# Kernel tuning notes

Hardware: AMD Instinct MI355X
Metric: run time of the kernel (lower is better)

Reference implementation:

```python
import jax, jax.numpy as jnp
import numpy as np

WS = 8          # window_size
HEADS = 8
HEAD_DIM = 32
DIM = 256
INNER = HEADS * HEAD_DIM  # 256
STRIDE = 2 * WS - 1       # 15


def _rel_idx_1d():
    # coords of the WS*WS pixels in a window
    coords = np.array([[x, y] for x in range(WS) for y in range(WS)], dtype=np.int32)
    rel = coords[None, :, :] - coords[:, None, :] + (WS - 1)   # [WS^2, WS^2, 2] in [0, 2WS-2]
    idx = rel[:, :, 0] * STRIDE + rel[:, :, 1]
    return jnp.asarray(np.clip(idx, 0, None).reshape(-1), dtype=jnp.int32)

_REL_IDX = _rel_idx_1d()  # [WS^2 * WS^2]


def setup_inputs() -> dict:
    key = jax.random.key(0)
    ks = jax.random.split(key, 5)
    b, l, H, W = 2, 4, 128, 128
    x = jax.random.normal(ks[0], (b, l, H, W, DIM), dtype=jnp.float32)
    W_qkv = jax.random.normal(ks[1], (DIM, 3 * INNER), dtype=jnp.float32) * (DIM ** -0.5)
    W_out = jax.random.normal(ks[2], (INNER, DIM), dtype=jnp.float32) * (INNER ** -0.5)
    b_out = jax.random.normal(ks[3], (DIM,), dtype=jnp.float32) * 0.02
    pos_emb = jax.random.normal(ks[4], (STRIDE, STRIDE), dtype=jnp.float32)
    return {"x": x, "W_qkv": W_qkv, "W_out": W_out, "b_out": b_out, "pos_emb": pos_emb}


def _to_windows(t, b, l, nh, nw):
    # [b,l,H,W,INNER] -> [b,l,heads,nh*nw,WS*WS,head_dim]
    t = t.reshape(b, l, nh, WS, nw, WS, HEADS, HEAD_DIM)
    t = t.transpose(0, 1, 6, 2, 4, 3, 5, 7)  # b l h nh nw ws ws d
    return t.reshape(b, l, HEADS, nh * nw, WS * WS, HEAD_DIM)


def reference(x, W_qkv, W_out, b_out, pos_emb):
    b, l, H, W, _ = x.shape
    nh, nw = H // WS, W // WS
    scale = HEAD_DIM ** -0.5

    qkv = x @ W_qkv                               # [b,l,H,W,3*INNER]
    q, k, v = jnp.split(qkv, 3, axis=-1)
    q = _to_windows(q, b, l, nh, nw)
    k = _to_windows(k, b, l, nh, nw)
    v = _to_windows(v, b, l, nh, nw)

    # per-window attention scores: [b,l,heads,windows,WS^2,WS^2]
    dots = jnp.einsum('blhwid,blhwjd->blhwij', q, k) * scale
    bias = pos_emb.reshape(-1)[_REL_IDX].reshape(WS * WS, WS * WS)
    dots = dots + bias

    attn = jax.nn.softmax(dots, axis=-1)
    out = jnp.einsum('blhwij,blhwjd->blhwid', attn, v)  # [b,l,heads,windows,WS^2,hd]

    # back to [b,l,H,W,INNER]
    out = out.reshape(b, l, HEADS, nh, nw, WS, WS, HEAD_DIM)
    out = out.transpose(0, 1, 3, 5, 4, 6, 2, 7)  # b l nh ws nw ws h d
    out = out.reshape(b, l, nh * WS, nw * WS, INNER)

    return out @ W_out + b_out  # dropout is identity at eval
```

## Files before the change

### kernel.cpp

```cpp
#include <hip/hip_runtime.h>
#include <hip/hip_bf16.h>

typedef short bf16x8 __attribute__((ext_vector_type(8)));
typedef float f32x4  __attribute__((ext_vector_type(4)));
typedef unsigned short u16;
typedef unsigned int u32;

#define MFMA16(a, b, c) __builtin_amdgcn_mfma_f32_16x16x32_bf16((a), (b), (c), 0, 0, 0)

static __device__ __forceinline__ u16 f2b(float f) {
  __hip_bfloat16 h = __float2bfloat16(f);
  return __builtin_bit_cast(u16, h);
}
static __device__ __forceinline__ float b2f(u16 v) {
  unsigned int u = ((unsigned int)v) << 16;
  return __builtin_bit_cast(float, u);
}
static __device__ __forceinline__ u32 pk2(float a, float b) {
  return (u32)f2b(a) | ((u32)f2b(b) << 16);
}

union FragU { uint4 u; bf16x8 v; };

static __device__ __forceinline__ bf16x8 shufx(uint2 lo, uint2 hi,
                                               int sA4, int sB4, bool uh) {
  u32 l0 = (u32)__builtin_amdgcn_ds_bpermute(sA4, (int)lo.x);
  u32 l1 = (u32)__builtin_amdgcn_ds_bpermute(sA4, (int)lo.y);
  u32 h0 = (u32)__builtin_amdgcn_ds_bpermute(sA4, (int)hi.x);
  u32 h1 = (u32)__builtin_amdgcn_ds_bpermute(sA4, (int)hi.y);
  u32 l2 = (u32)__builtin_amdgcn_ds_bpermute(sB4, (int)lo.x);
  u32 l3 = (u32)__builtin_amdgcn_ds_bpermute(sB4, (int)lo.y);
  u32 h2 = (u32)__builtin_amdgcn_ds_bpermute(sB4, (int)hi.x);
  u32 h3 = (u32)__builtin_amdgcn_ds_bpermute(sB4, (int)hi.y);
  FragU f;
  f.u.x = uh ? h0 : l0;  f.u.y = uh ? h1 : l1;
  f.u.z = uh ? h2 : l2;  f.u.w = uh ? h3 : l3;
  return f.v;
}

__global__ void prep(const float* __restrict__ wqkv, const float* __restrict__ wout,
                     const float* __restrict__ pos, u16* __restrict__ wqkT,
                     u16* __restrict__ wvB, u16* __restrict__ woutB,
                     u16* __restrict__ biasQ) {
  const int b = blockIdx.x, t = threadIdx.x;
  const float s = 0.17677669529663689f;
  if (b < 128) {
    int e0 = b * 1024 + t * 4;
#pragma unroll
    for (int i = 0; i < 4; ++i) {
      int e = e0 + i, o = e >> 8, ii = e & 255;
      float v = wqkv[(size_t)ii * 768 + o];
      wqkT[e] = f2b(o < 256 ? v * s : v);
    }
  } else if (b < 192) {
    int e0 = (b - 128) * 1024 + t * 4;
#pragma unroll
    for (int i = 0; i < 4; ++i) {
      int e = e0 + i, frag = e >> 9, w = e & 511, lane = w >> 3, ee = w & 7;
      int k8 = frag >> 4, np = frag & 15;
      int k = k8 * 32 + ((lane >> 4) << 3) + ee;
      int col = 512 + np * 16 + (lane & 15);
      wvB[e] = f2b(wqkv[(size_t)k * 768 + col]);
    }
  } else if (b < 256) {
    int e0 = (b - 192) * 1024 + t * 4;
#pragma unroll
    for (int i = 0; i < 4; ++i) {
      int e = e0 + i, frag = e >> 9, w = e & 511, lane = w >> 3, ee = w & 7;
      int k8 = frag >> 4, np = frag & 15;
      int k = k8 * 32 + ((lane >> 4) << 3) + ee;
      int col = np * 16 + (lane & 15);
      woutB[e] = f2b(wout[(size_t)k * 256 + col]);
    }
  } else {
    int e0 = (b - 256) * 1024 + t * 4;
#pragma unroll
    for (int i = 0; i < 4; ++i) {
      int e = e0 + i, iq = e >> 6, jk = e & 63;
      int ix = iq >> 3, iy = iq & 7, jx = jk >> 3, jy = jk & 7;
      biasQ[e] = f2b(pos[(jx - ix + 7) * 15 + (jy - iy + 7)]);
    }
  }
}

__global__ __launch_bounds__(512, 4)
void winattn(const float* __restrict__ x,
             const u16* __restrict__ wqkT,
             const u16* __restrict__ wvB,
             const u16* __restrict__ woutB,
             const float* __restrict__ b_out,
             const u16* __restrict__ biasQ,
             float* __restrict__ out) {
  __shared__ u16 Xs[64][264];
  __shared__ u16 WS[8][2304];
  __shared__ u16 Bs[64][68];

  const int tid  = threadIdx.x;
  const int lane = tid & 63;
  const int h    = tid >> 6;
  const int c    = lane & 15;
  const int g    = lane >> 4;

  u16* const ws = &WS[h][0];

  const int win = blockIdx.x;
  const int img = win >> 8;
  const int wid = win & 255;
  const int py0 = (wid >> 4) << 3;
  const int px0 = (wid & 15) << 3;
  const size_t imgbase = (size_t)img * (128 * 128);

  const f32x4 fz = {0.f, 0.f, 0.f, 0.f};

#pragma unroll
  for (int it = 0; it < 8; ++it) {
    int ch = tid + it * 512;
    int row = ch >> 6, c4 = (ch & 63) << 2;
    int py = py0 + (row >> 3), px = px0 + (row & 7);
    const float4 v = *reinterpret_cast<const float4*>(
        x + ((size_t)(imgbase + py * 128 + px)) * 256 + c4);
    ushort4 pk{f2b(v.x), f2b(v.y), f2b(v.z), f2b(v.w)};
    *reinterpret_cast<ushort4*>(&Xs[row][c4]) = pk;
  }
  {
    int row = tid >> 3, c0 = (tid & 7) * 8;
    *reinterpret_cast<ushort4*>(&Bs[row][c0]) =
        *reinterpret_cast<const ushort4*>(biasQ + row * 64 + c0);
    *reinterpret_cast<ushort4*>(&Bs[row][c0 + 4]) =
        *reinterpret_cast<const ushort4*>(biasQ + row * 64 + c0 + 4);
  }
  __syncthreads();

  const int sA4 = (c + 16 * ((2 * g) & 3)) * 4;
  const int sB4 = (c + 16 * ((2 * g + 1) & 3)) * 4;
  const bool uh = g >= 2;

  const int hq = h * 32, hk = 256 + h * 32;

  bf16x8 qf[4];
  {
    f32x4 aq[2][4];
#pragma unroll
    for (int mt = 0; mt < 2; ++mt)
#pragma unroll
      for (int nt = 0; nt < 4; ++nt) aq[mt][nt] = fz;
#pragma unroll 2
    for (int k8 = 0; k8 < 8; ++k8) {
      bf16x8 xb[4];
#pragma unroll
      for (int nt = 0; nt < 4; ++nt)
        xb[nt] = *reinterpret_cast<const bf16x8*>(&Xs[nt * 16 + c][k8 * 32 + g * 8]);
      bf16x8 wq[2];
#pragma unroll
      for (int mt = 0; mt < 2; ++mt)
        wq[mt] = *reinterpret_cast<const bf16x8*>(
            wqkT + (size_t)(hq + mt * 16 + c) * 256 + k8 * 32 + g * 8);
#pragma unroll
      for (int mt = 0; mt < 2; ++mt)
#pragma unroll
        for (int nt = 0; nt < 4; ++nt)
          aq[mt][nt] = MFMA16(wq[mt], xb[nt], aq[mt][nt]);
    }
#pragma unroll
    for (int nt = 0; nt < 4; ++nt)
#pragma unroll
      for (int mt = 0; mt < 2; ++mt) {
        uint2 pk{pk2(aq[mt][nt][0], aq[mt][nt][1]),
                 pk2(aq[mt][nt][2], aq[mt][nt][3])};
        *reinterpret_cast<uint2*>(&ws[(nt * 16 + c) * 36 + mt * 16 + 4 * g]) = pk;
      }
#pragma unroll
    for (int t4 = 0; t4 < 4; ++t4) {
      const u16* p = &ws[(t4 * 16 + c) * 36 + g * 8];
      uint2 a = *reinterpret_cast<const uint2*>(p);
      uint2 b = *reinterpret_cast<const uint2*>(p + 4);
      FragU f; f.u = uint4{a.x, a.y, b.x, b.y};
      qf[t4] = f.v;
    }
  }

  bf16x8 kf[4];
  {
    f32x4 ak[2][4];
#pragma unroll
    for (int mt = 0; mt < 2; ++mt)
#pragma unroll
      for (int nt = 0; nt < 4; ++nt) ak[mt][nt] = fz;
#pragma unroll 2
    for (int k8 = 0; k8 < 8; ++k8) {
      bf16x8 xb[4];
#pragma unroll
      for (int nt = 0; nt < 4; ++nt)
        xb[nt] = *reinterpret_cast<const bf16x8*>(&Xs[nt * 16 + c][k8 * 32 + g * 8]);
      bf16x8 wk[2];
#pragma unroll
      for (int mt = 0; mt < 2; ++mt)
        wk[mt] = *reinterpret_cast<const bf16x8*>(
            wqkT + (size_t)(hk + mt * 16 + c) * 256 + k8 * 32 + g * 8);
#pragma unroll
      for (int mt = 0; mt < 2; ++mt)
#pragma unroll
        for (int nt = 0; nt < 4; ++nt)
          ak[mt][nt] = MFMA16(wk[mt], xb[nt], ak[mt][nt]);
    }
#pragma unroll
    for (int nt = 0; nt < 4; ++nt)
#pragma unroll
      for (int mt = 0; mt < 2; ++mt) {
        uint2 pk{pk2(ak[mt][nt][0], ak[mt][nt][1]),
                 pk2(ak[mt][nt][2], ak[mt][nt][3])};
        *reinterpret_cast<uint2*>(&ws[(nt * 16 + c) * 36 + mt * 16 + 4 * g]) = pk;
      }
#pragma unroll
    for (int t4 = 0; t4 < 4; ++t4) {
      const u16* p = &ws[(t4 * 16 + c) * 36 + g * 8];
      uint2 a = *reinterpret_cast<const uint2*>(p);
      uint2 b = *reinterpret_cast<const uint2*>(p + 4);
      FragU f; f.u = uint4{a.x, a.y, b.x, b.y};
      kf[t4] = f.v;
    }
  }

  bf16x8 vf[2][2];
  {
    f32x4 av[4][2];
#pragma unroll
    for (int mt = 0; mt < 4; ++mt)
#pragma unroll
      for (int j = 0; j < 2; ++j) av[mt][j] = fz;
#pragma unroll 1
    for (int k8 = 0; k8 < 8; ++k8) {
      bf16x8 xb[4];
#pragma unroll
      for (int mt = 0; mt < 4; ++mt)
        xb[mt] = *reinterpret_cast<const bf16x8*>(&Xs[mt * 16 + c][k8 * 32 + g * 8]);
      bf16x8 bv[2];
#pragma unroll
      for (int j = 0; j < 2; ++j)
        bv[j] = *reinterpret_cast<const bf16x8*>(
            wvB + (size_t)((k8 * 16 + 2 * h + j) * 64 + lane) * 8);
#pragma unroll
      for (int mt = 0; mt < 4; ++mt)
#pragma unroll
        for (int j = 0; j < 2; ++j)
          av[mt][j] = MFMA16(xb[mt], bv[j], av[mt][j]);
    }
#pragma unroll
    for (int j = 0; j < 2; ++j)
#pragma unroll
      for (int mt = 0; mt < 4; ++mt) {
        uint2 pk{pk2(av[mt][j][0], av[mt][j][1]),
                 pk2(av[mt][j][2], av[mt][j][3])};
        *reinterpret_cast<uint2*>(&ws[(j * 16 + c) * 68 + mt * 16 + 4 * g]) = pk;
      }
#pragma unroll
    for (int kk = 0; kk < 2; ++kk)
#pragma unroll
      for (int dt = 0; dt < 2; ++dt) {
        const u16* p = &ws[(dt * 16 + c) * 68 + kk * 32 + g * 8];
        uint2 a = *reinterpret_cast<const uint2*>(p);
        uint2 b = *reinterpret_cast<const uint2*>(p + 4);
        FragU f; f.u = uint4{a.x, a.y, b.x, b.y};
        vf[kk][dt] = f.v;
      }
  }

  __builtin_amdgcn_s_setprio(1);
  ushort4 ao[8];
#pragma unroll
  for (int tqt = 0; tqt < 4; ++tqt) {
    f32x4 stq[4];
#pragma unroll
    for (int tkt = 0; tkt < 4; ++tkt) {
      const ushort4 bb = *reinterpret_cast<const ushort4*>(
          &Bs[tqt * 16 + c][tkt * 16 + 4 * g]);
      const f32x4 bf = {b2f(bb.x), b2f(bb.y), b2f(bb.z), b2f(bb.w)};
      stq[tkt] = MFMA16(kf[tkt], qf[tqt], bf);
    }
    float m0 = fmaxf(fmaxf(stq[0][0], stq[0][1]), fmaxf(stq[0][2], stq[0][3]));
    float m1 = fmaxf(fmaxf(stq[1][0], stq[1][1]), fmaxf(stq[1][2], stq[1][3]));
    float m2 = fmaxf(fmaxf(stq[2][0], stq[2][1]), fmaxf(stq[2][2], stq[2][3]));
    float m3 = fmaxf(fmaxf(stq[3][0], stq[3][1]), fmaxf(stq[3][2], stq[3][3]));
    float mx = fmaxf(fmaxf(m0, m1), fmaxf(m2, m3));
    mx = fmaxf(mx, __shfl_xor(mx, 16));
    mx = fmaxf(mx, __shfl_xor(mx, 32));
#pragma unroll
    for (int tkt = 0; tkt < 4; ++tkt)
#pragma unroll
      for (int r = 0; r < 4; ++r)
        stq[tkt][r] = __expf(stq[tkt][r] - mx);
    float s0 = (stq[0][0] + stq[0][1]) + (stq[0][2] + stq[0][3]);
    float s1 = (stq[1][0] + stq[1][1]) + (stq[1][2] + stq[1][3]);
    float s2 = (stq[2][0] + stq[2][1]) + (stq[2][2] + stq[2][3]);
    float s3 = (stq[3][0] + stq[3][1]) + (stq[3][2] + stq[3][3]);
    float sum = (s0 + s1) + (s2 + s3);
    sum += __shfl_xor(sum, 16);
    sum += __shfl_xor(sum, 32);
    const float rs = 1.0f / sum;

    f32x4 o0 = fz, o1 = fz;
#pragma unroll
    for (int kk = 0; kk < 2; ++kk) {
      uint2 lo{pk2(stq[2 * kk][0], stq[2 * kk][1]),
               pk2(stq[2 * kk][2], stq[2 * kk][3])};
      uint2 hi{pk2(stq[2 * kk + 1][0], stq[2 * kk + 1][1]),
               pk2(stq[2 * kk + 1][2], stq[2 * kk + 1][3])};
      bf16x8 pf = shufx(lo, hi, sA4, sB4, uh);
      o0 = MFMA16(vf[kk][0], pf, o0);
      o1 = MFMA16(vf[kk][1], pf, o1);
    }
    ao[tqt]     = ushort4{f2b(o0[0] * rs), f2b(o0[1] * rs),
                          f2b(o0[2] * rs), f2b(o0[3] * rs)};
    ao[4 + tqt] = ushort4{f2b(o1[0] * rs), f2b(o1[1] * rs),
                          f2b(o1[2] * rs), f2b(o1[3] * rs)};
  }
  __builtin_amdgcn_s_setprio(0);

  __syncthreads();
#pragma unroll
  for (int dt = 0; dt < 2; ++dt)
#pragma unroll
    for (int tqt = 0; tqt < 4; ++tqt)
      *reinterpret_cast<ushort4*>(&Xs[c + 16 * tqt][h * 32 + 16 * dt + 4 * g]) =
          ao[dt * 4 + tqt];
  __syncthreads();

  f32x4 yc[4][2];
#pragma unroll
  for (int mt = 0; mt < 4; ++mt)
#pragma unroll
    for (int jj = 0; jj < 2; ++jj) yc[mt][jj] = fz;
#pragma unroll 2
  for (int k8 = 0; k8 < 8; ++k8) {
    bf16x8 af[4];
#pragma unroll
    for (int mt = 0; mt < 4; ++mt)
      af[mt] = *reinterpret_cast<const bf16x8*>(&Xs[mt * 16 + c][k8 * 32 + g * 8]);
    bf16x8 bw[2];
#pragma unroll
    for (int jj = 0; jj < 2; ++jj) {
      int nt = h * 2 + jj;
      bw[jj] = *reinterpret_cast<const bf16x8*>(
          woutB + (size_t)((k8 * 16 + nt) * 64 + lane) * 8);
    }
#pragma unroll
    for (int mt = 0; mt < 4; ++mt)
#pragma unroll
      for (int jj = 0; jj < 2; ++jj)
        yc[mt][jj] = MFMA16(af[mt], bw[jj], yc[mt][jj]);
  }
#pragma unroll
  for (int jj = 0; jj < 2; ++jj) {
    const int nt = h * 2 + jj;
    const float bo = b_out[nt * 16 + c];
#pragma unroll
    for (int mt = 0; mt < 4; ++mt)
#pragma unroll
      for (int r = 0; r < 4; ++r) {
        int row = mt * 16 + g * 4 + r;
        int py = py0 + (row >> 3), px = px0 + (row & 7);
        out[((size_t)(imgbase + py * 128 + px)) * 256 + nt * 16 + c] =
            yc[mt][jj][r] + bo;
      }
  }
}

extern "C" void kernel_launch(void* const* d_in, const int* in_sizes, int n_in,
                              void* d_out, int out_size, void* d_ws, size_t ws_size,
                              hipStream_t stream) {
  const float* x    = (const float*)d_in[0];
  const float* wqkv = (const float*)d_in[1];
  const float* wout = (const float*)d_in[2];
  const float* bout = (const float*)d_in[3];
  const float* pos  = (const float*)d_in[4];
  float* out = (float*)d_out;

  u16* wqkT  = (u16*)d_ws;
  u16* wvB   = wqkT + 512 * 256;
  u16* woutB = wvB + 65536;
  u16* biasQ = woutB + 65536;

  prep<<<260, 256, 0, stream>>>(wqkv, wout, pos, wqkT, wvB, woutB, biasQ);
  winattn<<<2048, 512, 0, stream>>>(x, wqkT, wvB, woutB, bout, biasQ, out);
}
```

Measured before the change: 139.8 us.

## Process two windows per block and prefetch second window's input during attention

```diff
diff --git a/kernel.cpp b/kernel.cpp
--- a/kernel.cpp
+++ b/kernel.cpp
@@ -102,25 +102,23 @@
   const int g    = lane >> 4;
 
   u16* const ws = &WS[h][0];
-
-  const int win = blockIdx.x;
-  const int img = win >> 8;
-  const int wid = win & 255;
-  const int py0 = (wid >> 4) << 3;
-  const int px0 = (wid & 15) << 3;
-  const size_t imgbase = (size_t)img * (128 * 128);
-
   const f32x4 fz = {0.f, 0.f, 0.f, 0.f};
 
-#pragma unroll
-  for (int it = 0; it < 8; ++it) {
-    int ch = tid + it * 512;
-    int row = ch >> 6, c4 = (ch & 63) << 2;
-    int py = py0 + (row >> 3), px = px0 + (row & 7);
-    const float4 v = *reinterpret_cast<const float4*>(
-        x + ((size_t)(imgbase + py * 128 + px)) * 256 + c4);
-    ushort4 pk{f2b(v.x), f2b(v.y), f2b(v.z), f2b(v.w)};
-    *reinterpret_cast<ushort4*>(&Xs[row][c4]) = pk;
+  {
+    const int win = blockIdx.x;
+    const int img = win >> 8, wid = win & 255;
+    const int py0 = (wid >> 4) << 3, px0 = (wid & 15) << 3;
+    const size_t imgbase = (size_t)img * (128 * 128);
+#pragma unroll
+    for (int it = 0; it < 8; ++it) {
+      int ch = tid + it * 512;
+      int row = ch >> 6, c4 = (ch & 63) << 2;
+      int py = py0 + (row >> 3), px = px0 + (row & 7);
+      const float4 v = *reinterpret_cast<const float4*>(
+          x + (imgbase + py * 128 + px) * 256 + c4);
+      ushort4 pk{f2b(v.x), f2b(v.y), f2b(v.z), f2b(v.w)};
+      *reinterpret_cast<ushort4*>(&Xs[row][c4]) = pk;
+    }
   }
   {
     int row = tid >> 3, c0 = (tid & 7) * 8;
@@ -134,234 +132,270 @@
   const int sA4 = (c + 16 * ((2 * g) & 3)) * 4;
   const int sB4 = (c + 16 * ((2 * g + 1) & 3)) * 4;
   const bool uh = g >= 2;
-
   const int hq = h * 32, hk = 256 + h * 32;
 
-  bf16x8 qf[4];
-  {
-    f32x4 aq[2][4];
-#pragma unroll
-    for (int mt = 0; mt < 2; ++mt)
-#pragma unroll
-      for (int nt = 0; nt < 4; ++nt) aq[mt][nt] = fz;
+  float4 x2[8];
+
+#pragma unroll
+  for (int w = 0; w < 2; ++w) {
+    const int win = blockIdx.x + (w << 10);
+    const int img = win >> 8, wid = win & 255;
+    const int py0 = (wid >> 4) << 3, px0 = (wid & 15) << 3;
+    const size_t imgbase = (size_t)img * (128 * 128);
+
+    bf16x8 qf[4];
+    {
+      f32x4 aq[2][4];
+#pragma unroll
+      for (int mt = 0; mt < 2; ++mt)
+#pragma unroll
+        for (int nt = 0; nt < 4; ++nt) aq[mt][nt] = fz;
 #pragma unroll 2
-    for (int k8 = 0; k8 < 8; ++k8) {
-      bf16x8 xb[4];
+      for (int k8 = 0; k8 < 8; ++k8) {
+        bf16x8 xb[4];
+#pragma unroll
+        for (int nt = 0; nt < 4; ++nt)
+          xb[nt] = *reinterpret_cast<const bf16x8*>(&Xs[nt * 16 + c][k8 * 32 + g * 8]);
+        bf16x8 wq[2];
+#pragma unroll
+        for (int mt = 0; mt < 2; ++mt)
+          wq[mt] = *reinterpret_cast<const bf16x8*>(
+              wqkT + (size_t)(hq + mt * 16 + c) * 256 + k8 * 32 + g * 8);
+#pragma unroll
+        for (int mt = 0; mt < 2; ++mt)
+#pragma unroll
+          for (int nt = 0; nt < 4; ++nt)
+            aq[mt][nt] = MFMA16(wq[mt], xb[nt], aq[mt][nt]);
+      }
 #pragma unroll
       for (int nt = 0; nt < 4; ++nt)
-        xb[nt] = *reinterpret_cast<const bf16x8*>(&Xs[nt * 16 + c][k8 * 32 + g * 8]);
-      bf16x8 wq[2];
-#pragma unroll
-      for (int mt = 0; mt < 2; ++mt)
-        wq[mt] = *reinterpret_cast<const bf16x8*>(
-            wqkT + (size_t)(hq + mt * 16 + c) * 256 + k8 * 32 + g * 8);
-#pragma unroll
-      for (int mt = 0; mt < 2; ++mt)
-#pragma unroll
-        for (int nt = 0; nt < 4; ++nt)
-          aq[mt][nt] = MFMA16(wq[mt], xb[nt], aq[mt][nt]);
-    }
-#pragma unroll
-    for (int nt = 0; nt < 4; ++nt)
-#pragma unroll
-      for (int mt = 0; mt < 2; ++mt) {
-        uint2 pk{pk2(aq[mt][nt][0], aq[mt][nt][1]),
-                 pk2(aq[mt][nt][2], aq[mt][nt][3])};
-        *reinterpret_cast<uint2*>(&ws[(nt * 16 + c) * 36 + mt * 16 + 4 * g]) = pk;
-      }
-#pragma unroll
-    for (int t4 = 0; t4 < 4; ++t4) {
-      const u16* p = &ws[(t4 * 16 + c) * 36 + g * 8];
-      uint2 a = *reinterpret_cast<const uint2*>(p);
-      uint2 b = *reinterpret_cast<const uint2*>(p + 4);
-      FragU f; f.u = uint4{a.x, a.y, b.x, b.y};
-      qf[t4] = f.v;
-    }
-  }
-
-  bf16x8 kf[4];
-  {
-    f32x4 ak[2][4];
-#pragma unroll
-    for (int mt = 0; mt < 2; ++mt)
-#pragma unroll
-      for (int nt = 0; nt < 4; ++nt) ak[mt][nt] = fz;
-#pragma unroll 2
-    for (int k8 = 0; k8 < 8; ++k8) {
-      bf16x8 xb[4];
-#pragma unroll
-      for (int nt = 0; nt < 4; ++nt)
-        xb[nt] = *reinterpret_cast<const bf16x8*>(&Xs[nt * 16 + c][k8 * 32 + g * 8]);
-      bf16x8 wk[2];
-#pragma unroll
-      for (int mt = 0; mt < 2; ++mt)
-        wk[mt] = *reinterpret_cast<const bf16x8*>(
-            wqkT + (size_t)(hk + mt * 16 + c) * 256 + k8 * 32 + g * 8);
-#pragma unroll
-      for (int mt = 0; mt < 2; ++mt)
-#pragma unroll
-        for (int nt = 0; nt < 4; ++nt)
-          ak[mt][nt] = MFMA16(wk[mt], xb[nt], ak[mt][nt]);
-    }
-#pragma unroll
-    for (int nt = 0; nt < 4; ++nt)
-#pragma unroll
-      for (int mt = 0; mt < 2; ++mt) {
-        uint2 pk{pk2(ak[mt][nt][0], ak[mt][nt][1]),
-                 pk2(ak[mt][nt][2], ak[mt][nt][3])};
-        *reinterpret_cast<uint2*>(&ws[(nt * 16 + c) * 36 + mt * 16 + 4 * g]) = pk;
-      }
-#pragma unroll
-    for (int t4 = 0; t4 < 4; ++t4) {
-      const u16* p = &ws[(t4 * 16 + c) * 36 + g * 8];
-      uint2 a = *reinterpret_cast<const uint2*>(p);
-      uint2 b = *reinterpret_cast<const uint2*>(p + 4);
-      FragU f; f.u = uint4{a.x, a.y, b.x, b.y};
-      kf[t4] = f.v;
-    }
-  }
-
-  bf16x8 vf[2][2];
-  {
-    f32x4 av[4][2];
-#pragma unroll
-    for (int mt = 0; mt < 4; ++mt)
-#pragma unroll
-      for (int j = 0; j < 2; ++j) av[mt][j] = fz;
-#pragma unroll 1
-    for (int k8 = 0; k8 < 8; ++k8) {
-      bf16x8 xb[4];
-#pragma unroll
-      for (int mt = 0; mt < 4; ++mt)
-        xb[mt] = *reinterpret_cast<const bf16x8*>(&Xs[mt * 16 + c][k8 * 32 + g * 8]);
-      bf16x8 bv[2];
-#pragma unroll
-      for (int j = 0; j < 2; ++j)
-        bv[j] = *reinterpret_cast<const bf16x8*>(
-            wvB + (size_t)((k8 * 16 + 2 * h + j) * 64 + lane) * 8);
-#pragma unroll
-      for (int mt = 0; mt < 4; ++mt)
-#pragma unroll
-        for (int j = 0; j < 2; ++j)
-          av[mt][j] = MFMA16(xb[mt], bv[j], av[mt][j]);
-    }
-#pragma unroll
-    for (int j = 0; j < 2; ++j)
-#pragma unroll
-      for (int mt = 0; mt < 4; ++mt) {
-        uint2 pk{pk2(av[mt][j][0], av[mt][j][1]),
-                 pk2(av[mt][j][2], av[mt][j][3])};
-        *reinterpret_cast<uint2*>(&ws[(j * 16 + c) * 68 + mt * 16 + 4 * g]) = pk;
-      }
-#pragma unroll
-    for (int kk = 0; kk < 2; ++kk)
-#pragma unroll
-      for (int dt = 0; dt < 2; ++dt) {
-        const u16* p = &ws[(dt * 16 + c) * 68 + kk * 32 + g * 8];
+#pragma unroll
+        for (int mt = 0; mt < 2; ++mt) {
+          uint2 pk{pk2(aq[mt][nt][0], aq[mt][nt][1]),
+                   pk2(aq[mt][nt][2], aq[mt][nt][3])};
+          *reinterpret_cast<uint2*>(&ws[(nt * 16 + c) * 36 + mt * 16 + 4 * g]) = pk;
+        }
+#pragma unroll
+      for (int t4 = 0; t4 < 4; ++t4) {
+        const u16* p = &ws[(t4 * 16 + c) * 36 + g * 8];
         uint2 a = *reinterpret_cast<const uint2*>(p);
         uint2 b = *reinterpret_cast<const uint2*>(p + 4);
         FragU f; f.u = uint4{a.x, a.y, b.x, b.y};
-        vf[kk][dt] = f.v;
-      }
-  }
-
-  __builtin_amdgcn_s_setprio(1);
-  ushort4 ao[8];
-#pragma unroll
-  for (int tqt = 0; tqt < 4; ++tqt) {
-    f32x4 stq[4];
-#pragma unroll
-    for (int tkt = 0; tkt < 4; ++tkt) {
-      const ushort4 bb = *reinterpret_cast<const ushort4*>(
-          &Bs[tqt * 16 + c][tkt * 16 + 4 * g]);
-      const f32x4 bf = {b2f(bb.x), b2f(bb.y), b2f(bb.z), b2f(bb.w)};
-      stq[tkt] = MFMA16(kf[tkt], qf[tqt], bf);
-    }
-    float m0 = fmaxf(fmaxf(stq[0][0], stq[0][1]), fmaxf(stq[0][2], stq[0][3]));
-    float m1 = fmaxf(fmaxf(stq[1][0], stq[1][1]), fmaxf(stq[1][2], stq[1][3]));
-    float m2 = fmaxf(fmaxf(stq[2][0], stq[2][1]), fmaxf(stq[2][2], stq[2][3]));
-    float m3 = fmaxf(fmaxf(stq[3][0], stq[3][1]), fmaxf(stq[3][2], stq[3][3]));
-    float mx = fmaxf(fmaxf(m0, m1), fmaxf(m2, m3));
-    mx = fmaxf(mx, __shfl_xor(mx, 16));
-    mx = fmaxf(mx, __shfl_xor(mx, 32));
-#pragma unroll
-    for (int tkt = 0; tkt < 4; ++tkt)
-#pragma unroll
-      for (int r = 0; r < 4; ++r)
-        stq[tkt][r] = __expf(stq[tkt][r] - mx);
-    float s0 = (stq[0][0] + stq[0][1]) + (stq[0][2] + stq[0][3]);
-    float s1 = (stq[1][0] + stq[1][1]) + (stq[1][2] + stq[1][3]);
-    float s2 = (stq[2][0] + stq[2][1]) + (stq[2][2] + stq[2][3]);
-    float s3 = (stq[3][0] + stq[3][1]) + (stq[3][2] + stq[3][3]);
-    float sum = (s0 + s1) + (s2 + s3);
-    sum += __shfl_xor(sum, 16);
-    sum += __shfl_xor(sum, 32);
-    const float rs = 1.0f / sum;
-
-    f32x4 o0 = fz, o1 = fz;
-#pragma unroll
-    for (int kk = 0; kk < 2; ++kk) {
-      uint2 lo{pk2(stq[2 * kk][0], stq[2 * kk][1]),
-               pk2(stq[2 * kk][2], stq[2 * kk][3])};
-      uint2 hi{pk2(stq[2 * kk + 1][0], stq[2 * kk + 1][1]),
-               pk2(stq[2 * kk + 1][2], stq[2 * kk + 1][3])};
-      bf16x8 pf = shufx(lo, hi, sA4, sB4, uh);
-      o0 = MFMA16(vf[kk][0], pf, o0);
-      o1 = MFMA16(vf[kk][1], pf, o1);
-    }
-    ao[tqt]     = ushort4{f2b(o0[0] * rs), f2b(o0[1] * rs),
-                          f2b(o0[2] * rs), f2b(o0[3] * rs)};
-    ao[4 + tqt] = ushort4{f2b(o1[0] * rs), f2b(o1[1] * rs),
-                          f2b(o1[2] * rs), f2b(o1[3] * rs)};
-  }
-  __builtin_amdgcn_s_setprio(0);
-
-  __syncthreads();
-#pragma unroll
-  for (int dt = 0; dt < 2; ++dt)
-#pragma unroll
-    for (int tqt = 0; tqt < 4; ++tqt)
-      *reinterpret_cast<ushort4*>(&Xs[c + 16 * tqt][h * 32 + 16 * dt + 4 * g]) =
-          ao[dt * 4 + tqt];
-  __syncthreads();
-
-  f32x4 yc[4][2];
-#pragma unroll
-  for (int mt = 0; mt < 4; ++mt)
-#pragma unroll
-    for (int jj = 0; jj < 2; ++jj) yc[mt][jj] = fz;
+        qf[t4] = f.v;
+      }
+    }
+
+    bf16x8 kf[4];
+    {
+      f32x4 ak[2][4];
+#pragma unroll
+      for (int mt = 0; mt < 2; ++mt)
+#pragma unroll
+        for (int nt = 0; nt < 4; ++nt) ak[mt][nt] = fz;
 #pragma unroll 2
-  for (int k8 = 0; k8 < 8; ++k8) {
-    bf16x8 af[4];
+      for (int k8 = 0; k8 < 8; ++k8) {
+        bf16x8 xb[4];
+#pragma unroll
+        for (int nt = 0; nt < 4; ++nt)
+          xb[nt] = *reinterpret_cast<const bf16x8*>(&Xs[nt * 16 + c][k8 * 32 + g * 8]);
+        bf16x8 wk[2];
+#pragma unroll
+        for (int mt = 0; mt < 2; ++mt)
+          wk[mt] = *reinterpret_cast<const bf16x8*>(
+              wqkT + (size_t)(hk + mt * 16 + c) * 256 + k8 * 32 + g * 8);
+#pragma unroll
+        for (int mt = 0; mt < 2; ++mt)
+#pragma unroll
+          for (int nt = 0; nt < 4; ++nt)
+            ak[mt][nt] = MFMA16(wk[mt], xb[nt], ak[mt][nt]);
+      }
+#pragma unroll
+      for (int nt = 0; nt < 4; ++nt)
+#pragma unroll
+        for (int mt = 0; mt < 2; ++mt) {
+          uint2 pk{pk2(ak[mt][nt][0], ak[mt][nt][1]),
+                   pk2(ak[mt][nt][2], ak[mt][nt][3])};
+          *reinterpret_cast<uint2*>(&ws[(nt * 16 + c) * 36 + mt * 16 + 4 * g]) = pk;
+        }
+#pragma unroll
+      for (int t4 = 0; t4 < 4; ++t4) {
+        const u16* p = &ws[(t4 * 16 + c) * 36 + g * 8];
+        uint2 a = *reinterpret_cast<const uint2*>(p);
+        uint2 b = *reinterpret_cast<const uint2*>(p + 4);
+        FragU f; f.u = uint4{a.x, a.y, b.x, b.y};
+        kf[t4] = f.v;
+      }
+    }
+
+    bf16x8 vf[2][2];
+    {
+      f32x4 av[4][2];
+#pragma unroll
+      for (int mt = 0; mt < 4; ++mt)
+#pragma unroll
+        for (int j = 0; j < 2; ++j) av[mt][j] = fz;
+#pragma unroll 1
+      for (int k8 = 0; k8 < 8; ++k8) {
+        bf16x8 xb[4];
+#pragma unroll
+        for (int mt = 0; mt < 4; ++mt)
+          xb[mt] = *reinterpret_cast<const bf16x8*>(&Xs[mt * 16 + c][k8 * 32 + g * 8]);
+        bf16x8 bv[2];
+#pragma unroll
+        for (int j = 0; j < 2; ++j)
+          bv[j] = *reinterpret_cast<const bf16x8*>(
+              wvB + (size_t)((k8 * 16 + 2 * h + j) * 64 + lane) * 8);
+#pragma unroll
+        for (int mt = 0; mt < 4; ++mt)
+#pragma unroll
+          for (int j = 0; j < 2; ++j)
+            av[mt][j] = MFMA16(xb[mt], bv[j], av[mt][j]);
+      }
+#pragma unroll
+      for (int j = 0; j < 2; ++j)
+#pragma unroll
+        for (int mt = 0; mt < 4; ++mt) {
+          uint2 pk{pk2(av[mt][j][0], av[mt][j][1]),
+                   pk2(av[mt][j][2], av[mt][j][3])};
+          *reinterpret_cast<uint2*>(&ws[(j * 16 + c) * 68 + mt * 16 + 4 * g]) = pk;
+        }
+#pragma unroll
+      for (int kk = 0; kk < 2; ++kk)
+#pragma unroll
+        for (int dt = 0; dt < 2; ++dt) {
+          const u16* p = &ws[(dt * 16 + c) * 68 + kk * 32 + g * 8];
+          uint2 a = *reinterpret_cast<const uint2*>(p);
+          uint2 b = *reinterpret_cast<const uint2*>(p + 4);
+          FragU f; f.u = uint4{a.x, a.y, b.x, b.y};
+          vf[kk][dt] = f.v;
+        }
+    }
+
+    if (w == 0) {
+      const int win2 = blockIdx.x + 1024;
+      const int img2 = win2 >> 8, wid2 = win2 & 255;
+      const int py02 = (wid2 >> 4) << 3, px02 = (wid2 & 15) << 3;
+      const size_t base2 = (size_t)img2 * (128 * 128);
+#pragma unroll
+      for (int it = 0; it < 8; ++it) {
+        int ch = tid + it * 512;
+        int row = ch >> 6, c4 = (ch & 63) << 2;
+        int py = py02 + (row >> 3), px = px02 + (row & 7);
+        x2[it] = *reinterpret_cast<const float4*>(
+            x + (base2 + py * 128 + px) * 256 + c4);
+      }
+    }
+
+    __builtin_amdgcn_s_setprio(1);
+    ushort4 ao[8];
+#pragma unroll
+    for (int tqt = 0; tqt < 4; ++tqt) {
+      f32x4 stq[4];
+#pragma unroll
+      for (int tkt = 0; tkt < 4; ++tkt) {
+        const ushort4 bb = *reinterpret_cast<const ushort4*>(
+            &Bs[tqt * 16 + c][tkt * 16 + 4 * g]);
+        const f32x4 bf = {b2f(bb.x), b2f(bb.y), b2f(bb.z), b2f(bb.w)};
+        stq[tkt] = MFMA16(kf[tkt], qf[tqt], bf);
+      }
+      float m0 = fmaxf(fmaxf(stq[0][0], stq[0][1]), fmaxf(stq[0][2], stq[0][3]));
+      float m1 = fmaxf(fmaxf(stq[1][0], stq[1][1]), fmaxf(stq[1][2], stq[1][3]));
+      float m2 = fmaxf(fmaxf(stq[2][0], stq[2][1]), fmaxf(stq[2][2], stq[2][3]));
+      float m3 = fmaxf(fmaxf(stq[3][0], stq[3][1]), fmaxf(stq[3][2], stq[3][3]));
+      float mx = fmaxf(fmaxf(m0, m1), fmaxf(m2, m3));
+      mx = fmaxf(mx, __shfl_xor(mx, 16));
+      mx = fmaxf(mx, __shfl_xor(mx, 32));
+#pragma unroll
+      for (int tkt = 0; tkt < 4; ++tkt)
+#pragma unroll
+        for (int r = 0; r < 4; ++r)
+          stq[tkt][r] = __expf(stq[tkt][r] - mx);
+      float s0 = (stq[0][0] + stq[0][1]) + (stq[0][2] + stq[0][3]);
+      float s1 = (stq[1][0] + stq[1][1]) + (stq[1][2] + stq[1][3]);
+      float s2 = (stq[2][0] + stq[2][1]) + (stq[2][2] + stq[2][3]);
+      float s3 = (stq[3][0] + stq[3][1]) + (stq[3][2] + stq[3][3]);
+      float sum = (s0 + s1) + (s2 + s3);
+      sum += __shfl_xor(sum, 16);
+      sum += __shfl_xor(sum, 32);
+      const float rs = 1.0f / sum;
+
+      f32x4 o0 = fz, o1 = fz;
+#pragma unroll
+      for (int kk = 0; kk < 2; ++kk) {
+        uint2 lo{pk2(stq[2 * kk][0], stq[2 * kk][1]),
+                 pk2(stq[2 * kk][2], stq[2 * kk][3])};
+        uint2 hi{pk2(stq[2 * kk + 1][0], stq[2 * kk + 1][1]),
+                 pk2(stq[2 * kk + 1][2], stq[2 * kk + 1][3])};
+        bf16x8 pf = shufx(lo, hi, sA4, sB4, uh);
+        o0 = MFMA16(vf[kk][0], pf, o0);
+        o1 = MFMA16(vf[kk][1], pf, o1);
+      }
+      ao[tqt]     = ushort4{f2b(o0[0] * rs), f2b(o0[1] * rs),
+                            f2b(o0[2] * rs), f2b(o0[3] * rs)};
+      ao[4 + tqt] = ushort4{f2b(o1[0] * rs), f2b(o1[1] * rs),
+                            f2b(o1[2] * rs), f2b(o1[3] * rs)};
+    }
+    __builtin_amdgcn_s_setprio(0);
+
+    __syncthreads();
+#pragma unroll
+    for (int dt = 0; dt < 2; ++dt)
+#pragma unroll
+      for (int tqt = 0; tqt < 4; ++tqt)
+        *reinterpret_cast<ushort4*>(&Xs[c + 16 * tqt][h * 32 + 16 * dt + 4 * g]) =
+            ao[dt * 4 + tqt];
+    __syncthreads();
+
+    f32x4 yc[4][2];
 #pragma unroll
     for (int mt = 0; mt < 4; ++mt)
-      af[mt] = *reinterpret_cast<const bf16x8*>(&Xs[mt * 16 + c][k8 * 32 + g * 8]);
-    bf16x8 bw[2];
+#pragma unroll
+      for (int jj = 0; jj < 2; ++jj) yc[mt][jj] = fz;
+#pragma unroll 2
+    for (int k8 = 0; k8 < 8; ++k8) {
+      bf16x8 af[4];
+#pragma unroll
+      for (int mt = 0; mt < 4; ++mt)
+        af[mt] = *reinterpret_cast<const bf16x8*>(&Xs[mt * 16 + c][k8 * 32 + g * 8]);
+      bf16x8 bw[2];
+#pragma unroll
+      for (int jj = 0; jj < 2; ++jj) {
+        int nt = h * 2 + jj;
+        bw[jj] = *reinterpret_cast<const bf16x8*>(
+            woutB + (size_t)((k8 * 16 + nt) * 64 + lane) * 8);
+      }
+#pragma unroll
+      for (int mt = 0; mt < 4; ++mt)
+#pragma unroll
+        for (int jj = 0; jj < 2; ++jj)
+          yc[mt][jj] = MFMA16(af[mt], bw[jj], yc[mt][jj]);
+    }
 #pragma unroll
     for (int jj = 0; jj < 2; ++jj) {
-      int nt = h * 2 + jj;
-      bw[jj] = *reinterpret_cast<const bf16x8*>(
-          woutB + (size_t)((k8 * 16 + nt) * 64 + lane) * 8);
-    }
-#pragma unroll
-    for (int mt = 0; mt < 4; ++mt)
-#pragma unroll
-      for (int jj = 0; jj < 2; ++jj)
-        yc[mt][jj] = MFMA16(af[mt], bw[jj], yc[mt][jj]);
-  }
-#pragma unroll
-  for (int jj = 0; jj < 2; ++jj) {
-    const int nt = h * 2 + jj;
-    const float bo = b_out[nt * 16 + c];
-#pragma unroll
-    for (int mt = 0; mt < 4; ++mt)
-#pragma unroll
-      for (int r = 0; r < 4; ++r) {
-        int row = mt * 16 + g * 4 + r;
-        int py = py0 + (row >> 3), px = px0 + (row & 7);
-        out[((size_t)(imgbase + py * 128 + px)) * 256 + nt * 16 + c] =
-            yc[mt][jj][r] + bo;
-      }
+      const int nt = h * 2 + jj;
+      const float bo = b_out[nt * 16 + c];
+#pragma unroll
+      for (int mt = 0; mt < 4; ++mt)
+#pragma unroll
+        for (int r = 0; r < 4; ++r) {
+          int row = mt * 16 + g * 4 + r;
+          int py = py0 + (row >> 3), px = px0 + (row & 7);
+          out[(imgbase + py * 128 + px) * 256 + nt * 16 + c] =
+              yc[mt][jj][r] + bo;
+        }
+    }
+
+    if (w == 0) {
+      __syncthreads();
+#pragma unroll
+      for (int it = 0; it < 8; ++it) {
+        int ch = tid + it * 512;
+        int row = ch >> 6, c4 = (ch & 63) << 2;
+        ushort4 pk{f2b(x2[it].x), f2b(x2[it].y), f2b(x2[it].z), f2b(x2[it].w)};
+        *reinterpret_cast<ushort4*>(&Xs[row][c4]) = pk;
+      }
+      __syncthreads();
+    }
   }
 }
 
@@ -381,5 +415,5 @@
   u16* biasQ = woutB + 65536;
 
   prep<<<260, 256, 0, stream>>>(wqkv, wout, pos, wqkT, wvB, woutB, biasQ);
-  winattn<<<2048, 512, 0, stream>>>(x, wqkT, wvB, woutB, bout, biasQ, out);
-}
+  winattn<<<1024, 512, 0, stream>>>(x, wqkT, wvB, woutB, bout, biasQ, out);
+}
```

New measurement: 148.2 us. 6.1% more time.
